# Kernel optimization log

Hardware: AMD Instinct MI355X
Metric: run time of the kernel (lower is better)

The kernel has to match this reference:

```python
import jax, jax.numpy as jnp
import numpy as np

KERNEL_MUL = 2.0
KERNEL_NUM = 5


def _mmd(source, target, kernel_mul=KERNEL_MUL, kernel_num=KERNEL_NUM, fix_sigma=None):
    n = source.shape[0]
    total = jnp.concatenate([source, target], axis=0)  # [2N, D]
    n_samples = total.shape[0]
    # Pairwise squared L2 distances via Gram matrix (same math as the
    # broadcasted (2N,2N,D) diff-square-sum, but O(N^2 D) GEMM instead).
    sq = jnp.sum(total * total, axis=1)                # [2N]
    gram = total @ total.T                             # [2N, 2N]
    L2 = sq[:, None] + sq[None, :] - 2.0 * gram        # [2N, 2N]
    if fix_sigma:
        bandwidth = fix_sigma
    else:
        # torch used L2_distance.data -> detached; match with stop_gradient
        bandwidth = jax.lax.stop_gradient(jnp.sum(L2)) / (n_samples ** 2 - n_samples)
    bandwidth = bandwidth / (kernel_mul ** (kernel_num // 2))
    kernels = jnp.zeros_like(L2)
    for i in range(kernel_num):
        kernels = kernels + jnp.exp(-L2 / (bandwidth * kernel_mul ** i))
    XX = kernels[:n, :n]
    YY = kernels[n:, n:]
    XY = kernels[:n, n:]
    YX = kernels[n:, :n]
    return jnp.mean(XX + YY - XY - YX)


def setup_inputs() -> dict:
    key = jax.random.key(0)
    k1, k2 = jax.random.split(key)
    N, D = 4096, 512
    source = jax.random.normal(k1, (N, D), dtype=jnp.float32)
    target = jax.random.normal(k2, (N, D), dtype=jnp.float32)
    return {"source": source, "target": target}


def reference(source, target):
    # MMD_sample_size = inf >= batch_size -> single full-batch MMD
    return _mmd(source, target)
```

## Files before the change

kernel.cpp:

```cpp
#include <hip/hip_runtime.h>
#include <hip/hip_fp16.h>


#define NS 8192
#define D_DIM 512
#define NTILE 64

typedef _Float16 f16x8 __attribute__((ext_vector_type(8)));
typedef float f32x4 __attribute__((ext_vector_type(4)));

__global__ void prep_convert(const float* __restrict__ src, const float* __restrict__ tgt,
                             __half* __restrict__ Th, float* __restrict__ colsum) {
    int t = threadIdx.x;
    int r0 = blockIdx.x * 32;
    float c0 = 0.f, c1 = 0.f;
    for (int r = r0; r < r0 + 32; ++r) {
        const float* rowp = (r < 4096) ? (src + (size_t)r * D_DIM)
                                       : (tgt + (size_t)(r - 4096) * D_DIM);
        float2 v = *reinterpret_cast<const float2*>(rowp + 2 * t);
        __half h0 = __float2half(v.x), h1 = __float2half(v.y);
        __half2 hh; hh.x = h0; hh.y = h1;
        *reinterpret_cast<__half2*>(Th + (size_t)r * D_DIM + 2 * t) = hh;
        c0 += __half2float(h0); c1 += __half2float(h1);
    }
    atomicAdd(&colsum[2 * t], c0);
    atomicAdd(&colsum[2 * t + 1], c1);
}

__global__ void prep_sq(const __half* __restrict__ Th, float* __restrict__ sq) {
    int wid = threadIdx.x >> 6, lane = threadIdx.x & 63;
    int r = blockIdx.x * 4 + wid;
    const __half* rowp = Th + (size_t)r * D_DIM + lane * 8;
    int4 raw = *reinterpret_cast<const int4*>(rowp);
    const __half2* hp = reinterpret_cast<const __half2*>(&raw);
    float s = 0.f;
#pragma unroll
    for (int e = 0; e < 4; ++e) { float2 f = __half22float2(hp[e]); s += f.x * f.x + f.y * f.y; }
#pragma unroll
    for (int off = 32; off; off >>= 1) s += __shfl_xor(s, off, 64);
    if (lane == 0) sq[r] = s;
}

__global__ void compute_bw(const float* __restrict__ sq, const float* __restrict__ colsum,
                           float* __restrict__ cs5, double* __restrict__ acc) {
    __shared__ float red[256];
    int t = threadIdx.x;
    float s = 0.f;
    for (int i = t; i < NS; i += 256) s += sq[i];
    float c = 0.f;
    for (int i = t; i < D_DIM; i += 256) { float v = colsum[i]; c += v * v; }
    red[t] = s; __syncthreads();
    for (int off = 128; off; off >>= 1) { if (t < off) red[t] += red[t + off]; __syncthreads(); }
    float S = red[0]; __syncthreads();
    red[t] = c; __syncthreads();
    for (int off = 128; off; off >>= 1) { if (t < off) red[t] += red[t + off]; __syncthreads(); }
    if (t == 0) {
        float C = red[0];
        double sumL2 = 2.0 * (double)NS * (double)S - 2.0 * (double)C;
        double bw = sumL2 / ((double)NS * NS - (double)NS) / 4.0;
        for (int s5 = 0; s5 < 5; ++s5)
            cs5[s5] = (float)(-1.4426950408889634 / (bw * (double)(1 << s5)));
        *acc = 0.0;
    }
}

__global__ __launch_bounds__(256, 2) void mmd_main(const __half* __restrict__ Th,
                                                   const float* __restrict__ sq,
                                                   const float* __restrict__ cs5,
                                                   double* __restrict__ acc_out) {
    __shared__ __half Ah[128 * 32];
    __shared__ __half Bh[128 * 32];
    __shared__ float wred[4];

    int b = blockIdx.x;
    int ti = 0, rem = b;
    while (rem >= NTILE - ti) { rem -= NTILE - ti; ++ti; }
    int tj = ti + rem;
    int ibase = ti * 128, jbase = tj * 128;
    float wgt = ((ti == tj) ? 1.f : 2.f) * (((ti < 32) == (tj < 32)) ? 1.f : -1.f);

    int tid = threadIdx.x;
    int wid = tid >> 6, lane = tid & 63;
    int wm = wid >> 1, wn = wid & 1;

    f32x4 acc[4][4];
#pragma unroll
    for (int m = 0; m < 4; ++m)
#pragma unroll
        for (int n = 0; n < 4; ++n) acc[m][n] = f32x4{0.f, 0.f, 0.f, 0.f};

    for (int k0 = 0; k0 < D_DIM; k0 += 32) {
#pragma unroll
        for (int it = 0; it < 2; ++it) {
            int h = (tid + it * 256) * 8;
            int row = h >> 5, col = h & 31;
            __builtin_amdgcn_global_load_lds(
                (const __attribute__((address_space(1))) unsigned int*)(Th + (size_t)(ibase + row) * D_DIM + k0 + col),
                (__attribute__((address_space(3))) unsigned int*)(Ah + h), 16, 0, 0);
            __builtin_amdgcn_global_load_lds(
                (const __attribute__((address_space(1))) unsigned int*)(Th + (size_t)(jbase + row) * D_DIM + k0 + col),
                (__attribute__((address_space(3))) unsigned int*)(Bh + h), 16, 0, 0);
        }
        __syncthreads();

        f16x8 afr[4], bfr[4];
#pragma unroll
        for (int m = 0; m < 4; ++m)
            afr[m] = *reinterpret_cast<const f16x8*>(&Ah[(wm * 64 + m * 16 + (lane & 15)) * 32 + (lane >> 4) * 8]);
#pragma unroll
        for (int n = 0; n < 4; ++n)
            bfr[n] = *reinterpret_cast<const f16x8*>(&Bh[(wn * 64 + n * 16 + (lane & 15)) * 32 + (lane >> 4) * 8]);
#pragma unroll
        for (int m = 0; m < 4; ++m)
#pragma unroll
            for (int n = 0; n < 4; ++n)
                acc[m][n] = __builtin_amdgcn_mfma_f32_16x16x32_f16(afr[m], bfr[n], acc[m][n], 0, 0, 0);
        __syncthreads();
    }

    float sqi[16], sqj[4];
#pragma unroll
    for (int m = 0; m < 4; ++m)
#pragma unroll
        for (int r = 0; r < 4; ++r)
            sqi[m * 4 + r] = sq[ibase + wm * 64 + m * 16 + (lane >> 4) * 4 + r];
#pragma unroll
    for (int n = 0; n < 4; ++n)
        sqj[n] = sq[jbase + wn * 64 + n * 16 + (lane & 15)];
    float c[5];
#pragma unroll
    for (int s = 0; s < 5; ++s) c[s] = cs5[s];

    float ksum = 0.f;
#pragma unroll
    for (int m = 0; m < 4; ++m)
#pragma unroll
        for (int n = 0; n < 4; ++n)
#pragma unroll
            for (int r = 0; r < 4; ++r) {
                float L2 = sqi[m * 4 + r] + sqj[n] - 2.f * acc[m][n][r];
                ksum += __builtin_amdgcn_exp2f(L2 * c[0]) + __builtin_amdgcn_exp2f(L2 * c[1])
                      + __builtin_amdgcn_exp2f(L2 * c[2]) + __builtin_amdgcn_exp2f(L2 * c[3])
                      + __builtin_amdgcn_exp2f(L2 * c[4]);
            }
#pragma unroll
    for (int off = 32; off; off >>= 1) ksum += __shfl_xor(ksum, off, 64);
    if (lane == 0) wred[wid] = ksum;
    __syncthreads();
    if (tid == 0) {
        float tot = (wred[0] + wred[1]) + (wred[2] + wred[3]);
        atomicAdd(acc_out, (double)(tot * wgt));
    }
}

__global__ void finalize(const double* __restrict__ acc, float* __restrict__ out) {
    out[0] = (float)(*acc * (1.0 / (4096.0 * 4096.0)));
}

extern "C" void kernel_launch(void* const* d_in, const int* in_sizes, int n_in,
                              void* d_out, int out_size, void* d_ws, size_t ws_size,
                              hipStream_t stream) {
    (void)in_sizes; (void)n_in; (void)out_size; (void)ws_size;
    const float* src = (const float*)d_in[0];
    const float* tgt = (const float*)d_in[1];
    char* ws = (char*)d_ws;
    __half* Th    = (__half*)ws;
    float* sq     = (float*)(ws + 8388608);
    float* colsum = (float*)(ws + 8421376);
    float* cs5    = (float*)(ws + 8423424);
    double* acc   = (double*)(ws + 8423448);
    float* out    = (float*)d_out;

    hipMemsetAsync(colsum, 0, D_DIM * sizeof(float), stream);
    hipLaunchKernelGGL(prep_convert, dim3(256), dim3(256), 0, stream, src, tgt, Th, colsum);
    hipLaunchKernelGGL(prep_sq, dim3(NS / 4), dim3(256), 0, stream, Th, sq);
    hipLaunchKernelGGL(compute_bw, dim3(1), dim3(256), 0, stream, sq, colsum, cs5, acc);
    hipLaunchKernelGGL(mmd_main, dim3((NTILE * (NTILE + 1)) / 2), dim3(256), 0, stream, Th, sq, cs5, acc);
    hipLaunchKernelGGL(finalize, dim3(1), dim3(1), 0, stream, acc, out);
}
```

Before: 161.5 us.

## Fuse prep kernels, swizzle LDS, deepen K tile, replace exps with sqrt chain

The prep_convert and prep_sq kernels are merged into one pass that converts to fp16 and computes row norms and column sums. Column sums are reduced in shared memory before the atomics. The GEMM stage loads K=64 per step with an XOR-swizzled LDS layout to avoid bank conflicts, targets 4 blocks per SM, and remaps block IDs for XCD locality. In the epilogue the five exp2 calls per element become one exp2 plus four chained square roots, which relies on the bandwidths being powers of two; this adds some rounding error along the chain. The per-block LDS reduction is replaced with per-wave double atomics, which adds atomic traffic.

New measurement: 231.8 us. 43.5% more time.

```diff
diff --git a/kernel.cpp b/kernel.cpp
--- a/kernel.cpp
+++ b/kernel.cpp
@@ -5,44 +5,59 @@
 #define NS 8192
 #define D_DIM 512
 #define NTILE 64
+#define NBLK 2080
 
 typedef _Float16 f16x8 __attribute__((ext_vector_type(8)));
 typedef float f32x4 __attribute__((ext_vector_type(4)));
 
-__global__ void prep_convert(const float* __restrict__ src, const float* __restrict__ tgt,
-                             __half* __restrict__ Th, float* __restrict__ colsum) {
-    int t = threadIdx.x;
-    int r0 = blockIdx.x * 32;
-    float c0 = 0.f, c1 = 0.f;
-    for (int r = r0; r < r0 + 32; ++r) {
+__global__ __launch_bounds__(256) void prep(const float* __restrict__ src,
+                                            const float* __restrict__ tgt,
+                                            __half* __restrict__ Th,
+                                            float* __restrict__ sq,
+                                            float* __restrict__ colsum) {
+    __shared__ float lcs[4][D_DIM];
+    int tid = threadIdx.x, w = tid >> 6, l = tid & 63;
+    int r0 = blockIdx.x * 16 + w * 4;
+    float cs[8];
+#pragma unroll
+    for (int j = 0; j < 8; ++j) cs[j] = 0.f;
+
+#pragma unroll
+    for (int rr = 0; rr < 4; ++rr) {
+        int r = r0 + rr;
         const float* rowp = (r < 4096) ? (src + (size_t)r * D_DIM)
                                        : (tgt + (size_t)(r - 4096) * D_DIM);
-        float2 v = *reinterpret_cast<const float2*>(rowp + 2 * t);
-        __half h0 = __float2half(v.x), h1 = __float2half(v.y);
-        __half2 hh; hh.x = h0; hh.y = h1;
-        *reinterpret_cast<__half2*>(Th + (size_t)r * D_DIM + 2 * t) = hh;
-        c0 += __half2float(h0); c1 += __half2float(h1);
-    }
-    atomicAdd(&colsum[2 * t], c0);
-    atomicAdd(&colsum[2 * t + 1], c1);
-}
-
-__global__ void prep_sq(const __half* __restrict__ Th, float* __restrict__ sq) {
-    int wid = threadIdx.x >> 6, lane = threadIdx.x & 63;
-    int r = blockIdx.x * 4 + wid;
-    const __half* rowp = Th + (size_t)r * D_DIM + lane * 8;
-    int4 raw = *reinterpret_cast<const int4*>(rowp);
-    const __half2* hp = reinterpret_cast<const __half2*>(&raw);
-    float s = 0.f;
-#pragma unroll
-    for (int e = 0; e < 4; ++e) { float2 f = __half22float2(hp[e]); s += f.x * f.x + f.y * f.y; }
-#pragma unroll
-    for (int off = 32; off; off >>= 1) s += __shfl_xor(s, off, 64);
-    if (lane == 0) sq[r] = s;
+        float4 v0 = *reinterpret_cast<const float4*>(rowp + l * 8);
+        float4 v1 = *reinterpret_cast<const float4*>(rowp + l * 8 + 4);
+        float f[8] = {v0.x, v0.y, v0.z, v0.w, v1.x, v1.y, v1.z, v1.w};
+        __half h[8];
+        float s = 0.f;
+#pragma unroll
+        for (int j = 0; j < 8; ++j) {
+            h[j] = __float2half(f[j]);
+            float fj = __half2float(h[j]);
+            s += fj * fj;
+            cs[j] += fj;
+        }
+        *reinterpret_cast<int4*>(Th + (size_t)r * D_DIM + l * 8) =
+            *reinterpret_cast<const int4*>(h);
+#pragma unroll
+        for (int off = 32; off; off >>= 1) s += __shfl_xor(s, off, 64);
+        if (l == 0) sq[r] = s;
+    }
+#pragma unroll
+    for (int j = 0; j < 8; ++j) lcs[w][l * 8 + j] = cs[j];
+    __syncthreads();
+#pragma unroll
+    for (int j = 0; j < 2; ++j) {
+        int c = tid * 2 + j;
+        float v = (lcs[0][c] + lcs[1][c]) + (lcs[2][c] + lcs[3][c]);
+        atomicAdd(&colsum[c], v);
+    }
 }
 
 __global__ void compute_bw(const float* __restrict__ sq, const float* __restrict__ colsum,
-                           float* __restrict__ cs5, double* __restrict__ acc) {
+                           float* __restrict__ cs, double* __restrict__ acc) {
     __shared__ float red[256];
     int t = threadIdx.x;
     float s = 0.f;
@@ -58,21 +73,20 @@
         float C = red[0];
         double sumL2 = 2.0 * (double)NS * (double)S - 2.0 * (double)C;
         double bw = sumL2 / ((double)NS * NS - (double)NS) / 4.0;
-        for (int s5 = 0; s5 < 5; ++s5)
-            cs5[s5] = (float)(-1.4426950408889634 / (bw * (double)(1 << s5)));
+        cs[0] = (float)(-1.4426950408889634 / bw);
         *acc = 0.0;
     }
 }
 
-__global__ __launch_bounds__(256, 2) void mmd_main(const __half* __restrict__ Th,
+__global__ __launch_bounds__(256, 4) void mmd_main(const __half* __restrict__ Th,
                                                    const float* __restrict__ sq,
-                                                   const float* __restrict__ cs5,
+                                                   const float* __restrict__ cs,
                                                    double* __restrict__ acc_out) {
-    __shared__ __half Ah[128 * 32];
-    __shared__ __half Bh[128 * 32];
-    __shared__ float wred[4];
+    __shared__ __half Ah[128 * 64];
+    __shared__ __half Bh[128 * 64];
 
     int b = blockIdx.x;
+    b = (b & 7) * (NBLK / 8) + (b >> 3);
     int ti = 0, rem = b;
     while (rem >= NTILE - ti) { rem -= NTILE - ti; ++ti; }
     int tj = ti + rem;
@@ -82,6 +96,7 @@
     int tid = threadIdx.x;
     int wid = tid >> 6, lane = tid & 63;
     int wm = wid >> 1, wn = wid & 1;
+    int cl = lane >> 4;
 
     f32x4 acc[4][4];
 #pragma unroll
@@ -89,68 +104,76 @@
 #pragma unroll
         for (int n = 0; n < 4; ++n) acc[m][n] = f32x4{0.f, 0.f, 0.f, 0.f};
 
-    for (int k0 = 0; k0 < D_DIM; k0 += 32) {
-#pragma unroll
-        for (int it = 0; it < 2; ++it) {
-            int h = (tid + it * 256) * 8;
-            int row = h >> 5, col = h & 31;
+    for (int k0 = 0; k0 < D_DIM; k0 += 64) {
+#pragma unroll
+        for (int it = 0; it < 4; ++it) {
+            int h16 = tid + it * 256;
+            int row = h16 >> 3, ch = h16 & 7;
+            int scol = ((ch ^ (row & 7)) * 8);
             __builtin_amdgcn_global_load_lds(
-                (const __attribute__((address_space(1))) unsigned int*)(Th + (size_t)(ibase + row) * D_DIM + k0 + col),
-                (__attribute__((address_space(3))) unsigned int*)(Ah + h), 16, 0, 0);
+                (const __attribute__((address_space(1))) unsigned int*)(Th + (size_t)(ibase + row) * D_DIM + k0 + scol),
+                (__attribute__((address_space(3))) unsigned int*)(Ah + h16 * 8), 16, 0, 0);
             __builtin_amdgcn_global_load_lds(
-                (const __attribute__((address_space(1))) unsigned int*)(Th + (size_t)(jbase + row) * D_DIM + k0 + col),
-                (__attribute__((address_space(3))) unsigned int*)(Bh + h), 16, 0, 0);
+                (const __attribute__((address_space(1))) unsigned int*)(Th + (size_t)(jbase + row) * D_DIM + k0 + scol),
+                (__attribute__((address_space(3))) unsigned int*)(Bh + h16 * 8), 16, 0, 0);
         }
         __syncthreads();
 
-        f16x8 afr[4], bfr[4];
-#pragma unroll
-        for (int m = 0; m < 4; ++m)
-            afr[m] = *reinterpret_cast<const f16x8*>(&Ah[(wm * 64 + m * 16 + (lane & 15)) * 32 + (lane >> 4) * 8]);
+#pragma unroll
+        for (int ks = 0; ks < 2; ++ks) {
+            f16x8 afr[4], bfr[4];
+#pragma unroll
+            for (int m = 0; m < 4; ++m) {
+                int ra = wm * 64 + m * 16 + (lane & 15);
+                int pc = (ks * 4 + cl) ^ (ra & 7);
+                afr[m] = *reinterpret_cast<const f16x8*>(&Ah[ra * 64 + pc * 8]);
+            }
+#pragma unroll
+            for (int n = 0; n < 4; ++n) {
+                int rb = wn * 64 + n * 16 + (lane & 15);
+                int pc = (ks * 4 + cl) ^ (rb & 7);
+                bfr[n] = *reinterpret_cast<const f16x8*>(&Bh[rb * 64 + pc * 8]);
+            }
+#pragma unroll
+            for (int m = 0; m < 4; ++m)
+#pragma unroll
+                for (int n = 0; n < 4; ++n)
+                    acc[m][n] = __builtin_amdgcn_mfma_f32_16x16x32_f16(afr[m], bfr[n], acc[m][n], 0, 0, 0);
+        }
+        __syncthreads();
+    }
+
+    float c0 = cs[0];
+    float m2c0 = -2.f * c0;
+    float sci[16], scj[4];
+#pragma unroll
+    for (int m = 0; m < 4; ++m)
+#pragma unroll
+        for (int r = 0; r < 4; ++r)
+            sci[m * 4 + r] = sq[ibase + wm * 64 + m * 16 + (lane >> 4) * 4 + r] * c0;
+#pragma unroll
+    for (int n = 0; n < 4; ++n)
+        scj[n] = sq[jbase + wn * 64 + n * 16 + (lane & 15)] * c0;
+
+    float a0 = 0.f, a1 = 0.f, a2 = 0.f, a3 = 0.f, a4 = 0.f;
+#pragma unroll
+    for (int m = 0; m < 4; ++m)
 #pragma unroll
         for (int n = 0; n < 4; ++n)
-            bfr[n] = *reinterpret_cast<const f16x8*>(&Bh[(wn * 64 + n * 16 + (lane & 15)) * 32 + (lane >> 4) * 8]);
-#pragma unroll
-        for (int m = 0; m < 4; ++m)
-#pragma unroll
-            for (int n = 0; n < 4; ++n)
-                acc[m][n] = __builtin_amdgcn_mfma_f32_16x16x32_f16(afr[m], bfr[n], acc[m][n], 0, 0, 0);
-        __syncthreads();
-    }
-
-    float sqi[16], sqj[4];
-#pragma unroll
-    for (int m = 0; m < 4; ++m)
-#pragma unroll
-        for (int r = 0; r < 4; ++r)
-            sqi[m * 4 + r] = sq[ibase + wm * 64 + m * 16 + (lane >> 4) * 4 + r];
-#pragma unroll
-    for (int n = 0; n < 4; ++n)
-        sqj[n] = sq[jbase + wn * 64 + n * 16 + (lane & 15)];
-    float c[5];
-#pragma unroll
-    for (int s = 0; s < 5; ++s) c[s] = cs5[s];
-
-    float ksum = 0.f;
-#pragma unroll
-    for (int m = 0; m < 4; ++m)
-#pragma unroll
-        for (int n = 0; n < 4; ++n)
 #pragma unroll
             for (int r = 0; r < 4; ++r) {
-                float L2 = sqi[m * 4 + r] + sqj[n] - 2.f * acc[m][n][r];
-                ksum += __builtin_amdgcn_exp2f(L2 * c[0]) + __builtin_amdgcn_exp2f(L2 * c[1])
-                      + __builtin_amdgcn_exp2f(L2 * c[2]) + __builtin_amdgcn_exp2f(L2 * c[3])
-                      + __builtin_amdgcn_exp2f(L2 * c[4]);
+                float x0 = fmaf(acc[m][n][r], m2c0, sci[m * 4 + r] + scj[n]);
+                float e0 = __builtin_amdgcn_exp2f(x0);
+                float e1 = __builtin_amdgcn_sqrtf(e0);
+                float e2 = __builtin_amdgcn_sqrtf(e1);
+                float e3 = __builtin_amdgcn_sqrtf(e2);
+                float e4 = __builtin_amdgcn_sqrtf(e3);
+                a0 += e0; a1 += e1; a2 += e2; a3 += e3; a4 += e4;
             }
+    float ksum = ((a0 + a1) + (a2 + a3)) + a4;
 #pragma unroll
     for (int off = 32; off; off >>= 1) ksum += __shfl_xor(ksum, off, 64);
-    if (lane == 0) wred[wid] = ksum;
-    __syncthreads();
-    if (tid == 0) {
-        float tot = (wred[0] + wred[1]) + (wred[2] + wred[3]);
-        atomicAdd(acc_out, (double)(tot * wgt));
-    }
+    if (lane == 0) atomicAdd(acc_out, (double)(ksum * wgt));
 }
 
 __global__ void finalize(const double* __restrict__ acc, float* __restrict__ out) {
@@ -167,14 +190,13 @@
     __half* Th    = (__half*)ws;
     float* sq     = (float*)(ws + 8388608);
     float* colsum = (float*)(ws + 8421376);
-    float* cs5    = (float*)(ws + 8423424);
-    double* acc   = (double*)(ws + 8423448);
+    float* cs     = (float*)(ws + 8423424);
+    double* acc   = (double*)(ws + 8423432);
     float* out    = (float*)d_out;
 
     hipMemsetAsync(colsum, 0, D_DIM * sizeof(float), stream);
-    hipLaunchKernelGGL(prep_convert, dim3(256), dim3(256), 0, stream, src, tgt, Th, colsum);
-    hipLaunchKernelGGL(prep_sq, dim3(NS / 4), dim3(256), 0, stream, Th, sq);
-    hipLaunchKernelGGL(compute_bw, dim3(1), dim3(256), 0, stream, sq, colsum, cs5, acc);
-    hipLaunchKernelGGL(mmd_main, dim3((NTILE * (NTILE + 1)) / 2), dim3(256), 0, stream, Th, sq, cs5, acc);
+    hipLaunchKernelGGL(prep, dim3(512), dim3(256), 0, stream, src, tgt, Th, sq, colsum);
+    hipLaunchKernelGGL(compute_bw, dim3(1), dim3(256), 0, stream, sq, colsum, cs, acc);
+    hipLaunchKernelGGL(mmd_main, dim3(NBLK), dim3(256), 0, stream, Th, sq, cs, acc);
     hipLaunchKernelGGL(finalize, dim3(1), dim3(1), 0, stream, acc, out);
 }
```
